# Kernel tuning notes

Hardware: AMD Instinct MI355X
Metric: run time of the kernel (lower is better)

## Reference

```python
import jax, jax.numpy as jnp
import numpy as np

B, S, D, H, FF = 2, 2048, 512, 8, 2048
DK = D // H
EPS = 1e-3  # LayerNorm epsilon from the original module


def _layer_norm(x, gamma, beta):
    # biased variance over last dim, eps added inside sqrt (matches torch var_mean unbiased=False)
    mean = jnp.mean(x, axis=-1, keepdims=True)
    var = jnp.mean(jnp.square(x - mean), axis=-1, keepdims=True)
    return gamma * ((x - mean) / jnp.sqrt(var + EPS)) + beta


def setup_inputs() -> dict:
    key = jax.random.key(0)
    ks = jax.random.split(key, 16)
    sc = 0.02
    p = {
        'x': jax.random.normal(ks[0], (B, S, D), dtype=jnp.float32),
        'lengths': jax.random.randint(ks[1], (B,), 1, S + 1, dtype=jnp.int32),
        'Wq': jax.random.normal(ks[2], (D, D), dtype=jnp.float32) * sc,
        'bq': jnp.zeros((D,), dtype=jnp.float32),
        'Wk': jax.random.normal(ks[3], (D, D), dtype=jnp.float32) * sc,
        'bk': jnp.zeros((D,), dtype=jnp.float32),
        'Wv': jax.random.normal(ks[4], (D, D), dtype=jnp.float32) * sc,
        'bv': jnp.zeros((D,), dtype=jnp.float32),
        'Wo': jax.random.normal(ks[5], (D, D), dtype=jnp.float32) * sc,
        'bo': jnp.zeros((D,), dtype=jnp.float32),
        'W1': jax.random.normal(ks[6], (D, FF), dtype=jnp.float32) * sc,
        'b1': jnp.zeros((FF,), dtype=jnp.float32),
        'W2': jax.random.normal(ks[7], (FF, D), dtype=jnp.float32) * sc,
        'b2': jnp.zeros((D,), dtype=jnp.float32),
        'gamma1': jnp.ones((D,), dtype=jnp.float32),
        'beta1': jnp.zeros((D,), dtype=jnp.float32),
        'gamma2': jnp.ones((D,), dtype=jnp.float32),
        'beta2': jnp.zeros((D,), dtype=jnp.float32),
    }
    return p


def reference(x, lengths, Wq, bq, Wk, bk, Wv, bv, Wo, bo, W1, b1, W2, b2, gamma1, beta1, gamma2, beta2):
    neg_inf = jnp.float32(-jnp.inf)
    pos = jnp.arange(S)
    # pad mask: zero out padded token embeddings (create_pad_mask)
    pad = (pos[None, :] < lengths[:, None]).astype(x.dtype)  # (B, S)
    x = x * pad[:, :, None]

    # hand-rolled multi-head attention (NO 1/sqrt(d_k) scaling, matches original)
    q = (x @ Wq + bq).reshape(B, S, H, DK)
    k = (x @ Wk + bk).reshape(B, S, H, DK)
    v = (x @ Wv + bv).reshape(B, S, H, DK)
    scores = jnp.einsum('bshd,bqhd->bhsq', q, k)  # (B, H, S_query, S_key)

    # causal mask: key col j allowed iff j <= query row i
    causal = pos[None, :] <= pos[:, None]  # (S, S)
    # padding mask: key col j allowed iff j < lengths[b]
    keep = causal[None, None, :, :] & (pos[None, None, None, :] < lengths[:, None, None, None])
    scores = jnp.where(keep, scores, neg_inf)
    attn = jax.nn.softmax(scores, axis=-1)  # (B, H, S, S)

    # FAITHFUL to torch.einsum('bhss,bshd->bshd'): repeated 's' takes the DIAGONAL
    diag = jnp.einsum('bhss->bhs', attn)  # (B, H, S)
    weighted = diag.transpose(0, 2, 1)[:, :, :, None] * v  # (B, S, H, DK)
    attn_out = weighted.reshape(B, S, D) @ Wo + bo

    x = _layer_norm(x + attn_out, gamma1, beta1)
    ff = jax.nn.relu(x @ W1 + b1) @ W2 + b2  # dropout is identity in eval
    x = _layer_norm(x + ff, gamma2, beta2)
    return x
```

## Files before the change

### kernel.cpp

```cpp
#include <hip/hip_runtime.h>

#define B_   2
#define S_   2048
#define D_   512
#define H_   8
#define DK_  64
#define FF_  2048
#define EPS_ 1e-3f
#define QS_  1536

typedef __bf16 bf16;
typedef __bf16 bf16x4 __attribute__((ext_vector_type(4)));
typedef __bf16 bf16x8 __attribute__((ext_vector_type(8)));
typedef float  f32x4  __attribute__((ext_vector_type(4)));

struct Trans4Args {
  const float* w[4];
  bf16* thi[4];
  bf16* tlo[4];
  int rowOff[4];
};

__global__ __launch_bounds__(256) void transpose4_kernel(Trans4Args a) {
  __shared__ float tl[32][33];
  const int t = threadIdx.x;
  const int tx = t & 31, ty = t >> 5;
  const int n0 = blockIdx.x * 32, k0 = blockIdx.y * 32;
  const int wsel = blockIdx.z;
  const float* __restrict__ W = a.w[wsel];
#pragma unroll
  for (int r = 0; r < 32; r += 8)
    tl[r + ty][tx] = W[(size_t)(k0 + r + ty) * 512 + n0 + tx];
  __syncthreads();
  bf16* __restrict__ Thi = a.thi[wsel];
  bf16* __restrict__ Tlo = a.tlo[wsel];
  const int ro = a.rowOff[wsel];
#pragma unroll
  for (int r = 0; r < 32; r += 8) {
    const int n = r + ty;
    const float v = tl[tx][n];
    const bf16 h = (bf16)v;
    const size_t o = (size_t)(ro + n0 + n) * 512 + k0 + tx;
    Thi[o] = h;
    Tlo[o] = (bf16)(v - (float)h);
  }
}

__global__ __launch_bounds__(256) void transpose_split_kernel(
    const float* __restrict__ W, int K, int N,
    bf16* __restrict__ Thi, bf16* __restrict__ Tlo) {
  __shared__ float tl[32][33];
  const int t = threadIdx.x;
  const int tx = t & 31, ty = t >> 5;
  const int n0 = blockIdx.x * 32, k0 = blockIdx.y * 32;
#pragma unroll
  for (int r = 0; r < 32; r += 8)
    tl[r + ty][tx] = W[(size_t)(k0 + r + ty) * N + n0 + tx];
  __syncthreads();
#pragma unroll
  for (int r = 0; r < 32; r += 8) {
    const int n = r + ty;
    const float v = tl[tx][n];
    const bf16 h = (bf16)v;
    const size_t o = (size_t)(n0 + n) * K + k0 + tx;
    Thi[o] = h;
    Tlo[o] = (bf16)(v - (float)h);
  }
}

__global__ __launch_bounds__(256) void pack_bias_kernel(const float* __restrict__ bq,
                                                        const float* __restrict__ bk,
                                                        const float* __restrict__ bv,
                                                        float* __restrict__ out) {
  const int i = blockIdx.x * 256 + threadIdx.x;
  out[i] = (i < 512) ? bq[i] : (i < 1024) ? bk[i - 512] : bv[i - 1024];
}

__global__ __launch_bounds__(256) void mask_split_kernel(const float* __restrict__ x,
                                                         const int* __restrict__ lengths,
                                                         bf16* __restrict__ xhi,
                                                         bf16* __restrict__ xlo) {
  const int idx = blockIdx.x * 256 + threadIdx.x;
  const int d4 = D_ / 4;
  const int s = (idx / d4) & (S_ - 1);
  const int b = idx / (d4 * S_);
  float4 v = reinterpret_cast<const float4*>(x)[idx];
  if (s >= lengths[b]) { v.x = 0.f; v.y = 0.f; v.z = 0.f; v.w = 0.f; }
  const float vv[4] = {v.x, v.y, v.z, v.w};
  bf16x4 h, l;
#pragma unroll
  for (int c = 0; c < 4; ++c) {
    const bf16 hh = (bf16)vv[c];
    h[c] = hh;
    l[c] = (bf16)(vv[c] - (float)hh);
  }
  reinterpret_cast<bf16x4*>(xhi)[idx] = h;
  reinterpret_cast<bf16x4*>(xlo)[idx] = l;
}

enum { EPI_BIAS = 0, EPI_BIAS_RELU = 2, EPI_PART = 4 };

template <int EPI, bool SPLIT>
__global__ __launch_bounds__(256) void gemm_kernel(
    const bf16* __restrict__ Ahi, const bf16* __restrict__ Alo,
    const bf16* __restrict__ Bhi, const bf16* __restrict__ Blo,
    const float* __restrict__ bias,
    float* __restrict__ C, float* __restrict__ C2,
    bf16* __restrict__ Chi, bf16* __restrict__ Clo,
    int K, int ldc, int nx, int mn, int ksplit) {
  __shared__ __align__(16) bf16 As[2][64][40];
  __shared__ __align__(16) bf16 Bs[2][64][40];
  const int t = threadIdx.x;

  const int nwg = gridDim.x;
  const int chunk = nwg >> 3;
  const int virt = (blockIdx.x & 7) * chunk + (blockIdx.x >> 3);
  const int s = virt / mn;
  const int v2 = virt - s * mn;
  const int m0 = (v2 / nx) * 64, n0 = (v2 % nx) * 64;
  const int kb = s * ksplit;

  const int ar = t >> 2, ak = (t & 3) * 8;
  const int lane = t & 63, wv = t >> 6;
  const int wm = (wv >> 1) * 32, wn = (wv & 1) * 32;
  const int fr = lane & 15, fg = lane >> 4;

  f32x4 acc[2][2] = {};

  const bf16* pAhi = Ahi + (size_t)(m0 + ar) * K + kb + ak;
  const bf16* pAlo = Alo + (size_t)(m0 + ar) * K + kb + ak;
  const bf16* pBhi = Bhi + (size_t)(n0 + ar) * K + kb + ak;
  const bf16* pBlo = Blo + (size_t)(n0 + ar) * K + kb + ak;

  for (int k0 = 0; k0 < ksplit; k0 += 32) {
    *reinterpret_cast<int4*>(&As[0][ar][ak]) = *reinterpret_cast<const int4*>(pAhi + k0);
    *reinterpret_cast<int4*>(&As[1][ar][ak]) = *reinterpret_cast<const int4*>(pAlo + k0);
    *reinterpret_cast<int4*>(&Bs[0][ar][ak]) = *reinterpret_cast<const int4*>(pBhi + k0);
    *reinterpret_cast<int4*>(&Bs[1][ar][ak]) = *reinterpret_cast<const int4*>(pBlo + k0);
    __syncthreads();

    bf16x8 ah[2], al[2], bh[2], bl[2];
#pragma unroll
    for (int m = 0; m < 2; ++m) {
      ah[m] = *reinterpret_cast<const bf16x8*>(&As[0][wm + m * 16 + fr][fg * 8]);
      al[m] = *reinterpret_cast<const bf16x8*>(&As[1][wm + m * 16 + fr][fg * 8]);
      bh[m] = *reinterpret_cast<const bf16x8*>(&Bs[0][wn + m * 16 + fr][fg * 8]);
      bl[m] = *reinterpret_cast<const bf16x8*>(&Bs[1][wn + m * 16 + fr][fg * 8]);
    }
#pragma unroll
    for (int m = 0; m < 2; ++m)
#pragma unroll
      for (int n = 0; n < 2; ++n) {
        acc[m][n] = __builtin_amdgcn_mfma_f32_16x16x32_bf16(ah[m], bh[n], acc[m][n], 0, 0, 0);
        acc[m][n] = __builtin_amdgcn_mfma_f32_16x16x32_bf16(ah[m], bl[n], acc[m][n], 0, 0, 0);
        acc[m][n] = __builtin_amdgcn_mfma_f32_16x16x32_bf16(al[m], bh[n], acc[m][n], 0, 0, 0);
      }
    __syncthreads();
  }

  float* __restrict__ Cw = (s == 0) ? C : C2;
  float bcol[2] = {0.f, 0.f};
  if constexpr (EPI != EPI_PART) {
#pragma unroll
    for (int n = 0; n < 2; ++n) bcol[n] = bias[n0 + wn + n * 16 + fr];
  }
#pragma unroll
  for (int m = 0; m < 2; ++m)
#pragma unroll
    for (int n = 0; n < 2; ++n) {
      const int col = n0 + wn + n * 16 + fr;
#pragma unroll
      for (int r = 0; r < 4; ++r) {
        const int row = m0 + wm + m * 16 + fg * 4 + r;
        float v = acc[m][n][r] + bcol[n];
        if constexpr (EPI == EPI_BIAS_RELU) v = fmaxf(v, 0.f);
        const size_t o = (size_t)row * ldc + col;
        if constexpr (SPLIT) {
          const bf16 h = (bf16)v;
          Chi[o] = h;
          Clo[o] = (bf16)(v - (float)h);
        } else {
          Cw[o] = v;
        }
      }
    }
}

__global__ __launch_bounds__(256) void attn_part_kernel(const float* __restrict__ qkv,
                                                        const int* __restrict__ lengths,
                                                        float* __restrict__ pm,
                                                        float* __restrict__ pl,
                                                        float* __restrict__ pd) {
  __shared__ __align__(16) float Qs[64][68];
  __shared__ __align__(16) float Ks[64][68];
  const int t = threadIdx.x;
  const int tx = t & 15, ty = t >> 4;
  const int bh = blockIdx.y;
  const int bb = bh >> 3, h = bh & 7;

  const int p = blockIdx.x;
  int a = (int)sqrtf((float)p);
  while ((a + 1) * (a + 1) <= p) ++a;
  while (a * a > p) --a;
  int ib, jc;
  if (p >= a * a + a) { ib = 2 * a;     jc = p - (a * a + a); }
  else                { ib = 2 * a - 1; jc = p - a * a; }

  const int i0 = ib * 64;
  const int len = lengths[bb];
  if (i0 >= len || jc * 128 >= len) return;

  {
    const int r_ = t >> 4, quad = t & 15;
#pragma unroll
    for (int it = 0; it < 4; ++it) {
      const int r = it * 16 + r_;
      *reinterpret_cast<float4*>(&Qs[r][quad * 4]) = *reinterpret_cast<const float4*>(
          qkv + (size_t)(bb * S_ + i0 + r) * QS_ + h * DK_ + quad * 4);
    }
  }

  float m_r[4], l_r[4], d_r[4];
#pragma unroll
  for (int ii = 0; ii < 4; ++ii) { m_r[ii] = -1e30f; l_r[ii] = 0.f; d_r[ii] = 0.f; }

  const int jlim = min(i0 + 63, len - 1);
  for (int jt = 0; jt < 2; ++jt) {
    const int j0 = jc * 128 + jt * 64;
    if (j0 > jlim) break;
    {
      const int r_ = t >> 4, quad = t & 15;
#pragma unroll
      for (int it = 0; it < 4; ++it) {
        const int r = it * 16 + r_;
        *reinterpret_cast<float4*>(&Ks[r][quad * 4]) = *reinterpret_cast<const float4*>(
            qkv + (size_t)(bb * S_ + j0 + r) * QS_ + D_ + h * DK_ + quad * 4);
      }
    }
    __syncthreads();

    float sc[4][4] = {};
#pragma unroll 4
    for (int d0 = 0; d0 < 64; d0 += 4) {
      float4 qv[4], kv[4];
#pragma unroll
      for (int ii = 0; ii < 4; ++ii) qv[ii] = *reinterpret_cast<const float4*>(&Qs[ii * 16 + ty][d0]);
#pragma unroll
      for (int jj = 0; jj < 4; ++jj) kv[jj] = *reinterpret_cast<const float4*>(&Ks[jj * 16 + tx][d0]);
#pragma unroll
      for (int ii = 0; ii < 4; ++ii)
#pragma unroll
        for (int jj = 0; jj < 4; ++jj) {
          sc[ii][jj] = fmaf(qv[ii].x, kv[jj].x, sc[ii][jj]);
          sc[ii][jj] = fmaf(qv[ii].y, kv[jj].y, sc[ii][jj]);
          sc[ii][jj] = fmaf(qv[ii].z, kv[jj].z, sc[ii][jj]);
          sc[ii][jj] = fmaf(qv[ii].w, kv[jj].w, sc[ii][jj]);
        }
    }

#pragma unroll
    for (int ii = 0; ii < 4; ++ii) {
      const int ig = i0 + ii * 16 + ty;
      float mx = -1e30f;
#pragma unroll
      for (int jj = 0; jj < 4; ++jj) {
        const int j = j0 + jj * 16 + tx;
        if (j > ig || j >= len) sc[ii][jj] = -1e30f;
        mx = fmaxf(mx, sc[ii][jj]);
      }
#pragma unroll
      for (int off = 1; off < 16; off <<= 1) mx = fmaxf(mx, __shfl_xor(mx, off));
      const float mnew = fmaxf(m_r[ii], mx);
      float ps = 0.f, pdg = 0.f;
#pragma unroll
      for (int jj = 0; jj < 4; ++jj) {
        const int j = j0 + jj * 16 + tx;
        const float e = __expf(sc[ii][jj] - mnew);
        ps += e;
        if (j == ig) pdg = e;
      }
#pragma unroll
      for (int off = 1; off < 16; off <<= 1) {
        ps += __shfl_xor(ps, off);
        pdg += __shfl_xor(pdg, off);
      }
      const float scale = __expf(m_r[ii] - mnew);
      l_r[ii] = l_r[ii] * scale + ps;
      d_r[ii] = d_r[ii] * scale + pdg;
      m_r[ii] = mnew;
    }
    __syncthreads();
  }

  if (tx == 0) {
    const size_t base = ((size_t)(bh * 32 + ib) * 16 + jc) * 64;
#pragma unroll
    for (int ii = 0; ii < 4; ++ii) {
      const int row = ii * 16 + ty;
      const float mm = m_r[ii];
      const bool ok = mm > -1e29f;
      pm[base + row] = mm;
      pl[base + row] = ok ? l_r[ii] : 0.f;
      pd[base + row] = ok ? d_r[ii] : 0.f;
    }
  }
}

__global__ __launch_bounds__(256) void attn_merge_kernel(
    const float* __restrict__ qkv, const int* __restrict__ lengths,
    const float* __restrict__ pm, const float* __restrict__ pl,
    const float* __restrict__ pd, bf16* __restrict__ whi, bf16* __restrict__ wlo) {
  __shared__ float msh[4][64], lsh[4][64], dsh[4][64];
  __shared__ float dgs[64];
  const int t = threadIdx.x;
  const int ib = blockIdx.x, bh = blockIdx.y;
  const int bb = bh >> 3, h = bh & 7;
  const int i0 = ib * 64;
  const int len = lengths[bb];

  const int r = t & 63, g = t >> 6;
  float m = -1e30f, l = 0.f, d = 0.f;
  if (i0 < len) {
    const int jcmax = min((i0 + 63) >> 7, (len - 1) >> 7);
    const size_t base = ((size_t)(bh * 32 + ib) * 16) * 64 + r;
    for (int jc = g; jc <= jcmax; jc += 4) {
      const size_t idx = base + (size_t)jc * 64;
      const float m2 = pm[idx], l2 = pl[idx], d2 = pd[idx];
      const float mn = fmaxf(m, m2);
      const float e1 = __expf(m - mn), e2 = __expf(m2 - mn);
      l = l * e1 + l2 * e2;
      d = d * e1 + d2 * e2;
      m = mn;
    }
  }
  msh[g][r] = m; lsh[g][r] = l; dsh[g][r] = d;
  __syncthreads();
  if (t < 64) {
    float M = msh[0][t], L = lsh[0][t], Dv = dsh[0][t];
#pragma unroll
    for (int gg = 1; gg < 4; ++gg) {
      const float m2 = msh[gg][t], l2 = lsh[gg][t], d2 = dsh[gg][t];
      const float mn = fmaxf(M, m2);
      const float e1 = __expf(M - mn), e2 = __expf(m2 - mn);
      L = L * e1 + l2 * e2;
      Dv = Dv * e1 + d2 * e2;
      M = mn;
    }
    dgs[t] = (i0 + t < len) ? Dv / L : 0.f;
  }
  __syncthreads();

  const int rr = t >> 2, q = t & 3;
  const float dg = dgs[rr];
  const size_t vbase = (size_t)(bb * S_ + i0 + rr) * QS_ + 2 * D_ + h * DK_;
  const size_t obase = (size_t)(bb * S_ + i0 + rr) * D_ + h * DK_;
#pragma unroll
  for (int kk = 0; kk < 4; ++kk) {
    const int col = q * 4 + kk * 16;
    const float4 v4 = *reinterpret_cast<const float4*>(qkv + vbase + col);
    const float vv[4] = {dg * v4.x, dg * v4.y, dg * v4.z, dg * v4.w};
    bf16x4 hh, ll;
#pragma unroll
    for (int c = 0; c < 4; ++c) {
      const bf16 x = (bf16)vv[c];
      hh[c] = x;
      ll[c] = (bf16)(vv[c] - (float)x);
    }
    *reinterpret_cast<bf16x4*>(&whi[obase + col]) = hh;
    *reinterpret_cast<bf16x4*>(&wlo[obase + col]) = ll;
  }
}

__global__ __launch_bounds__(256) void ln1_fused_kernel(
    const float* __restrict__ P0, const float* __restrict__ P1,
    const float* __restrict__ x, const int* __restrict__ lengths,
    const float* __restrict__ bo,
    const float* __restrict__ gamma, const float* __restrict__ beta,
    bf16* __restrict__ Yhi, bf16* __restrict__ Ylo) {
  const int row = blockIdx.x;
  const int t = threadIdx.x;
  const int lenb = lengths[row >> 11];
  const bool valid = (row & (S_ - 1)) < lenb;
  const size_t ro = (size_t)row * D_ + t * 2;
  const float2 p0 = *reinterpret_cast<const float2*>(P0 + ro);
  const float2 p1 = *reinterpret_cast<const float2*>(P1 + ro);
  const float2 xv = *reinterpret_cast<const float2*>(x + ro);
  const float2 bv = *reinterpret_cast<const float2*>(bo + t * 2);
  float hx = p0.x + p1.x + bv.x + (valid ? xv.x : 0.f);
  float hy = p0.y + p1.y + bv.y + (valid ? xv.y : 0.f);

  float s = hx + hy, s2 = hx * hx + hy * hy;
#pragma unroll
  for (int off = 1; off < 64; off <<= 1) {
    s += __shfl_xor(s, off);
    s2 += __shfl_xor(s2, off);
  }
  __shared__ float red[8];
  const int w = t >> 6;
  if ((t & 63) == 0) { red[w] = s; red[4 + w] = s2; }
  __syncthreads();
  const float ts  = red[0] + red[1] + red[2] + red[3];
  const float ts2 = red[4] + red[5] + red[6] + red[7];
  const float mean = ts * (1.f / D_);
  const float var  = ts2 * (1.f / D_) - mean * mean;
  const float inv  = 1.f / sqrtf(var + EPS_);
  const float2 g  = *reinterpret_cast<const float2*>(gamma + t * 2);
  const float2 bt = *reinterpret_cast<const float2*>(beta + t * 2);
  const float ox = g.x * ((hx - mean) * inv) + bt.x;
  const float oy = g.y * ((hy - mean) * inv) + bt.y;
  const bf16 ohx = (bf16)ox, ohy = (bf16)oy;
  Yhi[ro] = ohx;  Yhi[ro + 1] = ohy;
  Ylo[ro] = (bf16)(ox - (float)ohx);
  Ylo[ro + 1] = (bf16)(oy - (float)ohy);
}

__global__ __launch_bounds__(256) void ln2_fused_kernel(
    const float* __restrict__ Q0, const float* __restrict__ Q1,
    const bf16* __restrict__ Yhi, const bf16* __restrict__ Ylo,
    const float* __restrict__ b2,
    const float* __restrict__ gamma, const float* __restrict__ beta,
    float* __restrict__ out) {
  const int row = blockIdx.x;
  const int t = threadIdx.x;
  const size_t ro = (size_t)row * D_ + t * 2;
  const float2 q0 = *reinterpret_cast<const float2*>(Q0 + ro);
  const float2 q1 = *reinterpret_cast<const float2*>(Q1 + ro);
  const float2 bv = *reinterpret_cast<const float2*>(b2 + t * 2);
  const float y1x = (float)Yhi[ro] + (float)Ylo[ro];
  const float y1y = (float)Yhi[ro + 1] + (float)Ylo[ro + 1];
  float hx = q0.x + q1.x + bv.x + y1x;
  float hy = q0.y + q1.y + bv.y + y1y;

  float s = hx + hy, s2 = hx * hx + hy * hy;
#pragma unroll
  for (int off = 1; off < 64; off <<= 1) {
    s += __shfl_xor(s, off);
    s2 += __shfl_xor(s2, off);
  }
  __shared__ float red[8];
  const int w = t >> 6;
  if ((t & 63) == 0) { red[w] = s; red[4 + w] = s2; }
  __syncthreads();
  const float ts  = red[0] + red[1] + red[2] + red[3];
  const float ts2 = red[4] + red[5] + red[6] + red[7];
  const float mean = ts * (1.f / D_);
  const float var  = ts2 * (1.f / D_) - mean * mean;
  const float inv  = 1.f / sqrtf(var + EPS_);
  const float2 g  = *reinterpret_cast<const float2*>(gamma + t * 2);
  const float2 bt = *reinterpret_cast<const float2*>(beta + t * 2);
  float2 o;
  o.x = g.x * ((hx - mean) * inv) + bt.x;
  o.y = g.y * ((hy - mean) * inv) + bt.y;
  *reinterpret_cast<float2*>(out + ro) = o;
}

extern "C" void kernel_launch(void* const* d_in, const int* in_sizes, int n_in,
                              void* d_out, int out_size, void* d_ws, size_t ws_size,
                              hipStream_t stream) {
  const float* x       = (const float*)d_in[0];
  const int*   lengths = (const int*)d_in[1];
  const float* Wq = (const float*)d_in[2];
  const float* bq = (const float*)d_in[3];
  const float* Wk = (const float*)d_in[4];
  const float* bk = (const float*)d_in[5];
  const float* Wv = (const float*)d_in[6];
  const float* bv = (const float*)d_in[7];
  const float* Wo = (const float*)d_in[8];
  const float* bo = (const float*)d_in[9];
  const float* W1 = (const float*)d_in[10];
  const float* b1 = (const float*)d_in[11];
  const float* W2 = (const float*)d_in[12];
  const float* b2 = (const float*)d_in[13];
  const float* gamma1 = (const float*)d_in[14];
  const float* beta1  = (const float*)d_in[15];
  const float* gamma2 = (const float*)d_in[16];
  const float* beta2  = (const float*)d_in[17];
  float* out = (float*)d_out;

  char* ws = (char*)d_ws;
  bf16*  qkvT_hi = (bf16*)(ws + 0);
  bf16*  qkvT_lo = (bf16*)(ws + 1572864);
  bf16*  WoT_hi  = (bf16*)(ws + 3145728);
  bf16*  WoT_lo  = (bf16*)(ws + 3670016);
  bf16*  W1T_hi  = (bf16*)(ws + 4194304);
  bf16*  W1T_lo  = (bf16*)(ws + 6291456);
  bf16*  W2T_hi  = (bf16*)(ws + 8388608);
  bf16*  W2T_lo  = (bf16*)(ws + 10485760);
  float* bqkv    = (float*)(ws + 12582912);
  float* qkv_f32 = (float*)(ws + 12589056);
  float* P0      = (float*)(ws + 12589056);
  float* P1      = (float*)(ws + 20977664);
  float* part_m  = (float*)(ws + 37754880);
  float* part_l  = (float*)(ws + 39852032);
  float* part_d  = (float*)(ws + 41949184);
  bf16*  ff1_hi  = (bf16*)(ws + 12589056);
  bf16*  ff1_lo  = (bf16*)(ws + 29366272);
  bf16*  xm_hi   = (bf16*)(ws + 46143488);
  bf16*  xm_lo   = (bf16*)(ws + 50337792);
  bf16*  y1_hi   = (bf16*)(ws + 46143488);
  bf16*  y1_lo   = (bf16*)(ws + 50337792);
  bf16*  wgt_hi  = (bf16*)(ws + 54532096);
  bf16*  wgt_lo  = (bf16*)(ws + 58726400);
  float* Q0      = (float*)(ws + 54532096);
  float* Q1      = (float*)(ws + 0);

  const dim3 blk(256);
  const int M = B_ * S_;

  Trans4Args ta;
  ta.w[0] = Wq; ta.w[1] = Wk; ta.w[2] = Wv; ta.w[3] = Wo;
  ta.thi[0] = qkvT_hi; ta.thi[1] = qkvT_hi; ta.thi[2] = qkvT_hi; ta.thi[3] = WoT_hi;
  ta.tlo[0] = qkvT_lo; ta.tlo[1] = qkvT_lo; ta.tlo[2] = qkvT_lo; ta.tlo[3] = WoT_lo;
  ta.rowOff[0] = 0; ta.rowOff[1] = 512; ta.rowOff[2] = 1024; ta.rowOff[3] = 0;
  transpose4_kernel<<<dim3(16, 16, 4), blk, 0, stream>>>(ta);
  transpose_split_kernel<<<dim3(64, 16), blk, 0, stream>>>(W1, 512, 2048, W1T_hi, W1T_lo);
  transpose_split_kernel<<<dim3(16, 64), blk, 0, stream>>>(W2, 2048, 512, W2T_hi, W2T_lo);
  pack_bias_kernel<<<dim3(6), blk, 0, stream>>>(bq, bk, bv, bqkv);

  mask_split_kernel<<<dim3((M * D_ / 4) / 256), blk, 0, stream>>>(x, lengths, xm_hi, xm_lo);

  gemm_kernel<EPI_BIAS, false><<<dim3(1536), blk, 0, stream>>>(
      xm_hi, xm_lo, qkvT_hi, qkvT_lo, bqkv,
      qkv_f32, nullptr, nullptr, nullptr, 512, QS_, 24, 1536, 512);

  attn_part_kernel<<<dim3(272, 16), blk, 0, stream>>>(qkv_f32, lengths, part_m, part_l, part_d);
  attn_merge_kernel<<<dim3(32, 16), blk, 0, stream>>>(qkv_f32, lengths, part_m, part_l, part_d,
                                                      wgt_hi, wgt_lo);

  gemm_kernel<EPI_PART, false><<<dim3(1024), blk, 0, stream>>>(
      wgt_hi, wgt_lo, WoT_hi, WoT_lo, nullptr,
      P0, P1, nullptr, nullptr, 512, D_, 8, 512, 256);

  ln1_fused_kernel<<<dim3(M), blk, 0, stream>>>(P0, P1, x, lengths, bo,
                                                gamma1, beta1, y1_hi, y1_lo);

  gemm_kernel<EPI_BIAS_RELU, true><<<dim3(2048), blk, 0, stream>>>(
      y1_hi, y1_lo, W1T_hi, W1T_lo, b1,
      nullptr, nullptr, ff1_hi, ff1_lo, 512, FF_, 32, 2048, 512);

  gemm_kernel<EPI_PART, false><<<dim3(1024), blk, 0, stream>>>(
      ff1_hi, ff1_lo, W2T_hi, W2T_lo, nullptr,
      Q0, Q1, nullptr, nullptr, FF_, D_, 8, 512, 1024);

  ln2_fused_kernel<<<dim3(M), blk, 0, stream>>>(Q0, Q1, y1_hi, y1_lo, b2,
                                                gamma2, beta2, out);
}
```

Before: 307.6 us.

## Move attention score computation to split-bf16 MFMA and emit Q/K pre-split from QKV GEMM

The attention partial kernel now computes QK^T scores with bf16 MFMA instructions using a hi/lo split (three products) instead of scalar fp32 FMAs. To feed it, the QKV GEMM gets a new epilogue that writes Q and K as bf16 hi/lo pairs and V as fp32 into separate buffers. The GEMM operand order is swapped so each lane holds four consecutive output columns, which allows vectorized bias loads and 4-wide stores. The main target is the scalar FMA cost of the score phase, plus narrower stores in the epilogues. The split-bf16 scores lose a little precision compared with fp32 because the lo*lo term is dropped, and the softmax has no scaling, which can amplify score errors.

```diff
diff --git a/kernel.cpp b/kernel.cpp
--- a/kernel.cpp
+++ b/kernel.cpp
@@ -98,7 +98,7 @@
   reinterpret_cast<bf16x4*>(xlo)[idx] = l;
 }
 
-enum { EPI_BIAS = 0, EPI_BIAS_RELU = 2, EPI_PART = 4 };
+enum { EPI_BIAS_RELU = 2, EPI_PART = 4, EPI_QKV = 5 };
 
 template <int EPI, bool SPLIT>
 __global__ __launch_bounds__(256) void gemm_kernel(
@@ -151,50 +151,70 @@
     for (int m = 0; m < 2; ++m)
 #pragma unroll
       for (int n = 0; n < 2; ++n) {
-        acc[m][n] = __builtin_amdgcn_mfma_f32_16x16x32_bf16(ah[m], bh[n], acc[m][n], 0, 0, 0);
-        acc[m][n] = __builtin_amdgcn_mfma_f32_16x16x32_bf16(ah[m], bl[n], acc[m][n], 0, 0, 0);
-        acc[m][n] = __builtin_amdgcn_mfma_f32_16x16x32_bf16(al[m], bh[n], acc[m][n], 0, 0, 0);
+        acc[m][n] = __builtin_amdgcn_mfma_f32_16x16x32_bf16(bh[n], ah[m], acc[m][n], 0, 0, 0);
+        acc[m][n] = __builtin_amdgcn_mfma_f32_16x16x32_bf16(bl[n], ah[m], acc[m][n], 0, 0, 0);
+        acc[m][n] = __builtin_amdgcn_mfma_f32_16x16x32_bf16(bh[n], al[m], acc[m][n], 0, 0, 0);
       }
     __syncthreads();
   }
 
   float* __restrict__ Cw = (s == 0) ? C : C2;
-  float bcol[2] = {0.f, 0.f};
-  if constexpr (EPI != EPI_PART) {
-#pragma unroll
-    for (int n = 0; n < 2; ++n) bcol[n] = bias[n0 + wn + n * 16 + fr];
-  }
-#pragma unroll
-  for (int m = 0; m < 2; ++m)
+#pragma unroll
+  for (int m = 0; m < 2; ++m) {
+    const int row = m0 + wm + m * 16 + fr;
 #pragma unroll
     for (int n = 0; n < 2; ++n) {
-      const int col = n0 + wn + n * 16 + fr;
-#pragma unroll
-      for (int r = 0; r < 4; ++r) {
-        const int row = m0 + wm + m * 16 + fg * 4 + r;
-        float v = acc[m][n][r] + bcol[n];
-        if constexpr (EPI == EPI_BIAS_RELU) v = fmaxf(v, 0.f);
-        const size_t o = (size_t)row * ldc + col;
-        if constexpr (SPLIT) {
-          const bf16 h = (bf16)v;
-          Chi[o] = h;
-          Clo[o] = (bf16)(v - (float)h);
+      const int col = n0 + wn + n * 16 + fg * 4;
+      f32x4 v = acc[m][n];
+      if constexpr (EPI != EPI_PART) {
+        const f32x4 b4 = *reinterpret_cast<const f32x4*>(bias + col);
+#pragma unroll
+        for (int c = 0; c < 4; ++c) v[c] += b4[c];
+      }
+      if constexpr (EPI == EPI_BIAS_RELU) {
+#pragma unroll
+        for (int c = 0; c < 4; ++c) v[c] = fmaxf(v[c], 0.f);
+      }
+      if constexpr (EPI == EPI_QKV) {
+        if (col < 1024) {
+          bf16x4 h, l;
+#pragma unroll
+          for (int c = 0; c < 4; ++c) {
+            const bf16 hh = (bf16)v[c];
+            h[c] = hh;
+            l[c] = (bf16)(v[c] - (float)hh);
+          }
+          *reinterpret_cast<bf16x4*>(&Chi[(size_t)row * 1024 + col]) = h;
+          *reinterpret_cast<bf16x4*>(&Clo[(size_t)row * 1024 + col]) = l;
         } else {
-          Cw[o] = v;
+          *reinterpret_cast<f32x4*>(&C[(size_t)row * D_ + col - 1024]) = v;
         }
-      }
-    }
-}
-
-__global__ __launch_bounds__(256) void attn_part_kernel(const float* __restrict__ qkv,
-                                                        const int* __restrict__ lengths,
-                                                        float* __restrict__ pm,
-                                                        float* __restrict__ pl,
-                                                        float* __restrict__ pd) {
-  __shared__ __align__(16) float Qs[64][68];
-  __shared__ __align__(16) float Ks[64][68];
-  const int t = threadIdx.x;
-  const int tx = t & 15, ty = t >> 4;
+      } else if constexpr (SPLIT) {
+        bf16x4 h, l;
+#pragma unroll
+        for (int c = 0; c < 4; ++c) {
+          const bf16 hh = (bf16)v[c];
+          h[c] = hh;
+          l[c] = (bf16)(v[c] - (float)hh);
+        }
+        *reinterpret_cast<bf16x4*>(&Chi[(size_t)row * ldc + col]) = h;
+        *reinterpret_cast<bf16x4*>(&Clo[(size_t)row * ldc + col]) = l;
+      } else {
+        *reinterpret_cast<f32x4*>(&Cw[(size_t)row * ldc + col]) = v;
+      }
+    }
+  }
+}
+
+__global__ __launch_bounds__(256) void attn_part_kernel(
+    const bf16* __restrict__ qk_hi, const bf16* __restrict__ qk_lo,
+    const int* __restrict__ lengths,
+    float* __restrict__ pm, float* __restrict__ pl, float* __restrict__ pd) {
+  __shared__ __align__(16) bf16 Qh[64][72], Ql[64][72];
+  __shared__ __align__(16) bf16 Kh[64][72], Kl[64][72];
+  const int t = threadIdx.x;
+  const int lane = t & 63, wv = t >> 6;
+  const int fr = lane & 15, fg = lane >> 4;
   const int bh = blockIdx.y;
   const int bb = bh >> 3, h = bh & 7;
 
@@ -210,104 +230,99 @@
   const int len = lengths[bb];
   if (i0 >= len || jc * 128 >= len) return;
 
+  const int sr = t >> 2, sc0 = (t & 3) * 16;
   {
-    const int r_ = t >> 4, quad = t & 15;
-#pragma unroll
-    for (int it = 0; it < 4; ++it) {
-      const int r = it * 16 + r_;
-      *reinterpret_cast<float4*>(&Qs[r][quad * 4]) = *reinterpret_cast<const float4*>(
-          qkv + (size_t)(bb * S_ + i0 + r) * QS_ + h * DK_ + quad * 4);
-    }
+    const size_t gb = (size_t)(bb * S_ + i0 + sr) * 1024 + h * DK_ + sc0;
+    *reinterpret_cast<int4*>(&Qh[sr][sc0])     = *reinterpret_cast<const int4*>(qk_hi + gb);
+    *reinterpret_cast<int4*>(&Qh[sr][sc0 + 8]) = *reinterpret_cast<const int4*>(qk_hi + gb + 8);
+    *reinterpret_cast<int4*>(&Ql[sr][sc0])     = *reinterpret_cast<const int4*>(qk_lo + gb);
+    *reinterpret_cast<int4*>(&Ql[sr][sc0 + 8]) = *reinterpret_cast<const int4*>(qk_lo + gb + 8);
   }
 
   float m_r[4], l_r[4], d_r[4];
 #pragma unroll
-  for (int ii = 0; ii < 4; ++ii) { m_r[ii] = -1e30f; l_r[ii] = 0.f; d_r[ii] = 0.f; }
+  for (int r = 0; r < 4; ++r) { m_r[r] = -1e30f; l_r[r] = 0.f; d_r[r] = 0.f; }
 
   const int jlim = min(i0 + 63, len - 1);
   for (int jt = 0; jt < 2; ++jt) {
     const int j0 = jc * 128 + jt * 64;
     if (j0 > jlim) break;
     {
-      const int r_ = t >> 4, quad = t & 15;
-#pragma unroll
-      for (int it = 0; it < 4; ++it) {
-        const int r = it * 16 + r_;
-        *reinterpret_cast<float4*>(&Ks[r][quad * 4]) = *reinterpret_cast<const float4*>(
-            qkv + (size_t)(bb * S_ + j0 + r) * QS_ + D_ + h * DK_ + quad * 4);
-      }
+      const size_t gb = (size_t)(bb * S_ + j0 + sr) * 1024 + 512 + h * DK_ + sc0;
+      *reinterpret_cast<int4*>(&Kh[sr][sc0])     = *reinterpret_cast<const int4*>(qk_hi + gb);
+      *reinterpret_cast<int4*>(&Kh[sr][sc0 + 8]) = *reinterpret_cast<const int4*>(qk_hi + gb + 8);
+      *reinterpret_cast<int4*>(&Kl[sr][sc0])     = *reinterpret_cast<const int4*>(qk_lo + gb);
+      *reinterpret_cast<int4*>(&Kl[sr][sc0 + 8]) = *reinterpret_cast<const int4*>(qk_lo + gb + 8);
     }
     __syncthreads();
 
-    float sc[4][4] = {};
-#pragma unroll 4
-    for (int d0 = 0; d0 < 64; d0 += 4) {
-      float4 qv[4], kv[4];
-#pragma unroll
-      for (int ii = 0; ii < 4; ++ii) qv[ii] = *reinterpret_cast<const float4*>(&Qs[ii * 16 + ty][d0]);
-#pragma unroll
-      for (int jj = 0; jj < 4; ++jj) kv[jj] = *reinterpret_cast<const float4*>(&Ks[jj * 16 + tx][d0]);
-#pragma unroll
-      for (int ii = 0; ii < 4; ++ii)
-#pragma unroll
-        for (int jj = 0; jj < 4; ++jj) {
-          sc[ii][jj] = fmaf(qv[ii].x, kv[jj].x, sc[ii][jj]);
-          sc[ii][jj] = fmaf(qv[ii].y, kv[jj].y, sc[ii][jj]);
-          sc[ii][jj] = fmaf(qv[ii].z, kv[jj].z, sc[ii][jj]);
-          sc[ii][jj] = fmaf(qv[ii].w, kv[jj].w, sc[ii][jj]);
-        }
-    }
-
-#pragma unroll
-    for (int ii = 0; ii < 4; ++ii) {
-      const int ig = i0 + ii * 16 + ty;
+    f32x4 sc[4] = {};
+#pragma unroll
+    for (int kk = 0; kk < 2; ++kk) {
+      const bf16x8 qh = *reinterpret_cast<const bf16x8*>(&Qh[wv * 16 + fr][kk * 32 + fg * 8]);
+      const bf16x8 ql = *reinterpret_cast<const bf16x8*>(&Ql[wv * 16 + fr][kk * 32 + fg * 8]);
+#pragma unroll
+      for (int jf = 0; jf < 4; ++jf) {
+        const bf16x8 kh = *reinterpret_cast<const bf16x8*>(&Kh[jf * 16 + fr][kk * 32 + fg * 8]);
+        const bf16x8 kl = *reinterpret_cast<const bf16x8*>(&Kl[jf * 16 + fr][kk * 32 + fg * 8]);
+        sc[jf] = __builtin_amdgcn_mfma_f32_16x16x32_bf16(qh, kh, sc[jf], 0, 0, 0);
+        sc[jf] = __builtin_amdgcn_mfma_f32_16x16x32_bf16(qh, kl, sc[jf], 0, 0, 0);
+        sc[jf] = __builtin_amdgcn_mfma_f32_16x16x32_bf16(ql, kh, sc[jf], 0, 0, 0);
+      }
+    }
+
+#pragma unroll
+    for (int r = 0; r < 4; ++r) {
+      const int ig = i0 + wv * 16 + fg * 4 + r;
+      float s4[4];
       float mx = -1e30f;
 #pragma unroll
-      for (int jj = 0; jj < 4; ++jj) {
-        const int j = j0 + jj * 16 + tx;
-        if (j > ig || j >= len) sc[ii][jj] = -1e30f;
-        mx = fmaxf(mx, sc[ii][jj]);
+      for (int jf = 0; jf < 4; ++jf) {
+        const int j = j0 + jf * 16 + fr;
+        float v = sc[jf][r];
+        if (j > ig || j >= len) v = -1e30f;
+        s4[jf] = v;
+        mx = fmaxf(mx, v);
       }
 #pragma unroll
       for (int off = 1; off < 16; off <<= 1) mx = fmaxf(mx, __shfl_xor(mx, off));
-      const float mnew = fmaxf(m_r[ii], mx);
+      const float mnew = fmaxf(m_r[r], mx);
       float ps = 0.f, pdg = 0.f;
 #pragma unroll
-      for (int jj = 0; jj < 4; ++jj) {
-        const int j = j0 + jj * 16 + tx;
-        const float e = __expf(sc[ii][jj] - mnew);
+      for (int jf = 0; jf < 4; ++jf) {
+        const float e = __expf(s4[jf] - mnew);
         ps += e;
-        if (j == ig) pdg = e;
+        if (j0 + jf * 16 + fr == ig) pdg = e;
       }
 #pragma unroll
       for (int off = 1; off < 16; off <<= 1) {
         ps += __shfl_xor(ps, off);
         pdg += __shfl_xor(pdg, off);
       }
-      const float scale = __expf(m_r[ii] - mnew);
-      l_r[ii] = l_r[ii] * scale + ps;
-      d_r[ii] = d_r[ii] * scale + pdg;
-      m_r[ii] = mnew;
+      const float scale = __expf(m_r[r] - mnew);
+      l_r[r] = l_r[r] * scale + ps;
+      d_r[r] = d_r[r] * scale + pdg;
+      m_r[r] = mnew;
     }
     __syncthreads();
   }
 
-  if (tx == 0) {
+  if (fr == 0) {
     const size_t base = ((size_t)(bh * 32 + ib) * 16 + jc) * 64;
 #pragma unroll
-    for (int ii = 0; ii < 4; ++ii) {
-      const int row = ii * 16 + ty;
-      const float mm = m_r[ii];
+    for (int r = 0; r < 4; ++r) {
+      const int row = wv * 16 + fg * 4 + r;
+      const float mm = m_r[r];
       const bool ok = mm > -1e29f;
       pm[base + row] = mm;
-      pl[base + row] = ok ? l_r[ii] : 0.f;
-      pd[base + row] = ok ? d_r[ii] : 0.f;
+      pl[base + row] = ok ? l_r[r] : 0.f;
+      pd[base + row] = ok ? d_r[r] : 0.f;
     }
   }
 }
 
 __global__ __launch_bounds__(256) void attn_merge_kernel(
-    const float* __restrict__ qkv, const int* __restrict__ lengths,
+    const float* __restrict__ vsrc, const int* __restrict__ lengths,
     const float* __restrict__ pm, const float* __restrict__ pl,
     const float* __restrict__ pd, bf16* __restrict__ whi, bf16* __restrict__ wlo) {
   __shared__ float msh[4][64], lsh[4][64], dsh[4][64];
@@ -352,12 +367,11 @@
 
   const int rr = t >> 2, q = t & 3;
   const float dg = dgs[rr];
-  const size_t vbase = (size_t)(bb * S_ + i0 + rr) * QS_ + 2 * D_ + h * DK_;
   const size_t obase = (size_t)(bb * S_ + i0 + rr) * D_ + h * DK_;
 #pragma unroll
   for (int kk = 0; kk < 4; ++kk) {
     const int col = q * 4 + kk * 16;
-    const float4 v4 = *reinterpret_cast<const float4*>(qkv + vbase + col);
+    const float4 v4 = *reinterpret_cast<const float4*>(vsrc + obase + col);
     const float vv[4] = {dg * v4.x, dg * v4.y, dg * v4.z, dg * v4.w};
     bf16x4 hh, ll;
 #pragma unroll
@@ -487,7 +501,9 @@
   bf16*  W2T_hi  = (bf16*)(ws + 8388608);
   bf16*  W2T_lo  = (bf16*)(ws + 10485760);
   float* bqkv    = (float*)(ws + 12582912);
-  float* qkv_f32 = (float*)(ws + 12589056);
+  bf16*  qk_hi   = (bf16*)(ws + 12589056);
+  bf16*  qk_lo   = (bf16*)(ws + 20977664);
+  float* v_f32   = (float*)(ws + 29366272);
   float* P0      = (float*)(ws + 12589056);
   float* P1      = (float*)(ws + 20977664);
   float* part_m  = (float*)(ws + 37754880);
@@ -519,12 +535,13 @@
 
   mask_split_kernel<<<dim3((M * D_ / 4) / 256), blk, 0, stream>>>(x, lengths, xm_hi, xm_lo);
 
-  gemm_kernel<EPI_BIAS, false><<<dim3(1536), blk, 0, stream>>>(
+  gemm_kernel<EPI_QKV, false><<<dim3(1536), blk, 0, stream>>>(
       xm_hi, xm_lo, qkvT_hi, qkvT_lo, bqkv,
-      qkv_f32, nullptr, nullptr, nullptr, 512, QS_, 24, 1536, 512);
-
-  attn_part_kernel<<<dim3(272, 16), blk, 0, stream>>>(qkv_f32, lengths, part_m, part_l, part_d);
-  attn_merge_kernel<<<dim3(32, 16), blk, 0, stream>>>(qkv_f32, lengths, part_m, part_l, part_d,
+      v_f32, nullptr, qk_hi, qk_lo, 512, QS_, 24, 1536, 512);
+
+  attn_part_kernel<<<dim3(272, 16), blk, 0, stream>>>(qk_hi, qk_lo, lengths,
+                                                      part_m, part_l, part_d);
+  attn_merge_kernel<<<dim3(32, 16), blk, 0, stream>>>(v_f32, lengths, part_m, part_l, part_d,
                                                       wgt_hi, wgt_lo);
 
   gemm_kernel<EPI_PART, false><<<dim3(1024), blk, 0, stream>>>(
```

Measured after the change: 286.2 us. 7.0% less time.
